# Optimization experiments

Hardware: AMD Instinct MI355X
Metric: run time of the kernel (lower is better)

Reference implementation:

```python
import jax, jax.numpy as jnp
import numpy as np

N_NODES = 100000
N_EDGES = 1600000
D_FEAT = 128
D_OUT = 128


def gcn_conv(x, W, b, src, dst, w, n):
    # symmetric normalization (PyG GCNConv with self-loops already appended)
    deg = jax.ops.segment_sum(w, dst, num_segments=n)
    dinv = jnp.where(deg > 0, jax.lax.rsqrt(deg), 0.0)
    norm = dinv[src] * w * dinv[dst]                       # [E]
    h = x @ W                                              # [N, Dout]
    out = jax.ops.segment_sum(h[src] * norm[:, None], dst, num_segments=n)
    return out + b


def setup_inputs() -> dict:
    key = jax.random.key(0)
    ks = jax.random.split(key, 20)
    feat = jax.random.normal(ks[0], (N_NODES, D_FEAT), dtype=jnp.float32)
    gdv = jax.random.uniform(ks[1], (N_NODES, 73), dtype=jnp.float32)
    pr = jax.random.uniform(ks[2], (N_NODES, 1), dtype=jnp.float32)
    edge_index = jax.random.randint(ks[3], (2, N_EDGES), 0, N_NODES, dtype=jnp.int32)
    edge_weight = jax.random.uniform(ks[4], (N_EDGES,), dtype=jnp.float32)

    def lin(k, fi, fo):
        bound = 1.0 / np.sqrt(fi)
        k1, k2 = jax.random.split(k)
        W = jax.random.uniform(k1, (fi, fo), minval=-bound, maxval=bound, dtype=jnp.float32)
        b = jax.random.uniform(k2, (fo,), minval=-bound, maxval=bound, dtype=jnp.float32)
        return W, b

    W1, b1 = lin(ks[5], D_FEAT, D_OUT)          # gcn_layer1
    W2, b2 = lin(ks[6], D_OUT, D_OUT // 2)      # gcn_layer2
    gdv_W, gdv_b = lin(ks[7], 73, D_OUT // 4)
    pr_W, pr_b = lin(ks[8], 1, D_OUT // 4)
    enc_W1, enc_b1 = lin(ks[9], D_OUT, D_OUT)
    enc_W2, enc_b2 = lin(ks[10], D_OUT, D_OUT)
    return dict(feat=feat, gdv=gdv, pr=pr, edge_index=edge_index, edge_weight=edge_weight,
                W1=W1, b1=b1, W2=W2, b2=b2, gdv_W=gdv_W, gdv_b=gdv_b, pr_W=pr_W, pr_b=pr_b,
                enc_W1=enc_W1, enc_b1=enc_b1, enc_W2=enc_W2, enc_b2=enc_b2)


def reference(feat, gdv, pr, edge_index, edge_weight,
              W1, b1, W2, b2, gdv_W, gdv_b, pr_W, pr_b,
              enc_W1, enc_b1, enc_W2, enc_b2):
    n = feat.shape[0]
    loop = jnp.arange(n, dtype=edge_index.dtype)
    src = jnp.concatenate([edge_index[0], loop])
    dst = jnp.concatenate([edge_index[1], loop])
    w = jnp.concatenate([edge_weight, jnp.ones((n,), dtype=edge_weight.dtype)])

    h = jnp.tanh(gcn_conv(feat, W1, b1, src, dst, w, n))
    adj = jax.nn.sigmoid(gcn_conv(h, W2, b2, src, dst, w, n))   # [N, D/2]

    g = jax.nn.sigmoid(gdv @ gdv_W + gdv_b)                      # [N, D/4]
    p = jax.nn.sigmoid(pr @ pr_W + pr_b)                         # [N, D/4]

    enc = jnp.concatenate([adj, g, p], axis=1)                   # [N, D]
    enc = jnp.tanh(enc @ enc_W1 + enc_b1) @ enc_W2 + enc_b2
    return enc
```

## Files before the change

kernel.cpp:

```cpp
#include <hip/hip_runtime.h>
#include <hip/hip_bf16.h>
#include <cstdint>
#include <cstddef>

#define TPB 256
#define SCAN_CHUNK 1024

typedef short bf16x8 __attribute__((ext_vector_type(8)));
typedef float f32x4 __attribute__((ext_vector_type(4)));

__device__ __forceinline__ float sigmoidf_(float x) {
    return 1.0f / (1.0f + __expf(-x));
}
__device__ __forceinline__ unsigned short f2bf(float x) {
    unsigned u = __float_as_uint(x);
    u += 0x7FFF + ((u >> 16) & 1);
    return (unsigned short)(u >> 16);
}
__device__ __forceinline__ float bf2f(unsigned short b) {
    return __uint_as_float(((unsigned)b) << 16);
}

__device__ __forceinline__ void gld_lds16(const void* gsrc, void* ldst) {
    __builtin_amdgcn_global_load_lds(
        (const __attribute__((address_space(1))) unsigned*)gsrc,
        (__attribute__((address_space(3))) unsigned*)ldst, 16, 0, 0);
}


__global__ __launch_bounds__(TPB) void k_zero(unsigned* counts, int n) {
    int i = blockIdx.x * TPB + threadIdx.x;
    if (i < n) counts[i] = 0u;
}

__global__ __launch_bounds__(TPB) void k_pass1(const int* __restrict__ dst,
                                               unsigned* __restrict__ counts,
                                               unsigned* __restrict__ epos, int E) {
    int e = blockIdx.x * TPB + threadIdx.x;
    if (e < E) epos[e] = atomicAdd(&counts[dst[e]], 1u);
}

__global__ __launch_bounds__(TPB) void k_scan_a(const unsigned* __restrict__ counts,
                                                int* __restrict__ rowptr,
                                                int* __restrict__ bsums, int n) {
    __shared__ int s[SCAN_CHUNK];
    int base = blockIdx.x * SCAN_CHUNK;
    int orig[4];
    #pragma unroll
    for (int j0 = 0; j0 < 4; ++j0) {
        int j = threadIdx.x + j0 * TPB;
        int v = (base + j < n) ? (int)counts[base + j] : 0;
        orig[j0] = v;
        s[j] = v;
    }
    __syncthreads();
    for (int off = 1; off < SCAN_CHUNK; off <<= 1) {
        int t[4];
        #pragma unroll
        for (int j0 = 0; j0 < 4; ++j0) {
            int j = threadIdx.x + j0 * TPB;
            t[j0] = (j >= off) ? s[j - off] : 0;
        }
        __syncthreads();
        #pragma unroll
        for (int j0 = 0; j0 < 4; ++j0) {
            int j = threadIdx.x + j0 * TPB;
            s[j] += t[j0];
        }
        __syncthreads();
    }
    #pragma unroll
    for (int j0 = 0; j0 < 4; ++j0) {
        int j = threadIdx.x + j0 * TPB;
        if (base + j < n) rowptr[base + j] = s[j] - orig[j0];
    }
    if (threadIdx.x == 0) bsums[blockIdx.x] = s[SCAN_CHUNK - 1];
}

__global__ void k_scan_b(int* bsums, int nb) {
    __shared__ int s[128];
    int t = threadIdx.x;
    int v = (t < nb) ? bsums[t] : 0;
    s[t] = v;
    __syncthreads();
    for (int off = 1; off < 128; off <<= 1) {
        int x = (t >= off) ? s[t - off] : 0;
        __syncthreads();
        s[t] += x;
        __syncthreads();
    }
    if (t < nb) bsums[t] = s[t] - v;
}

__global__ __launch_bounds__(TPB) void k_scan_c(int* __restrict__ rowptr,
                                                const int* __restrict__ bsums,
                                                int n, int E) {
    int i = blockIdx.x * TPB + threadIdx.x;
    if (i < n) rowptr[i] += bsums[i / SCAN_CHUNK];
    if (i == 0) rowptr[n] = E;
}

__global__ __launch_bounds__(TPB) void k_fill(const int* __restrict__ src,
                                              const int* __restrict__ dst,
                                              const float* __restrict__ ew,
                                              const int* __restrict__ rowptr,
                                              const unsigned* __restrict__ epos,
                                              int* __restrict__ colIdx,
                                              float* __restrict__ valNorm, int E) {
    int e = blockIdx.x * TPB + threadIdx.x;
    if (e < E) {
        unsigned slot = (unsigned)rowptr[dst[e]] + epos[e];
        colIdx[slot] = src[e];
        valNorm[slot] = ew[e];
    }
}

__global__ __launch_bounds__(TPB) void k_deg(const int* __restrict__ rowptr,
                                             const float* __restrict__ valRaw,
                                             float* __restrict__ dinv, int n) {
    int i = blockIdx.x * TPB + threadIdx.x;
    if (i >= n) return;
    int beg = rowptr[i], end = rowptr[i + 1];
    float s = 1.0f;
    for (int e = beg; e < end; ++e) s += valRaw[e];
    dinv[i] = rsqrtf(s);
}

__global__ __launch_bounds__(TPB) void k_scale(const int* __restrict__ colIdx,
                                               const float* __restrict__ dinv,
                                               float* __restrict__ valNorm, int E) {
    int e = blockIdx.x * TPB + threadIdx.x;
    if (e < E) valNorm[e] *= dinv[colIdx[e]];
}

template<int D, int ACT>
__global__ __launch_bounds__(TPB) void k_agg(const unsigned short* __restrict__ h,
                                             const int* __restrict__ rowptr,
                                             const int* __restrict__ colIdx,
                                             const float* __restrict__ valNorm,
                                             const float* __restrict__ dinv,
                                             const float* __restrict__ bias,
                                             unsigned short* __restrict__ out,
                                             int ldo, int n) {
    const int lane = threadIdx.x & 63;
    const int node = blockIdx.x * 4 + (threadIdx.x >> 6);
    if (node >= n) return;
    constexpr int PER = D / 64;
    float acc[PER];
    const float di = dinv[node];
    if constexpr (PER == 2) {
        unsigned hv = *(const unsigned*)&h[(size_t)node * D + lane * 2];
        acc[0] = bf2f((unsigned short)hv) * di;
        acc[1] = bf2f((unsigned short)(hv >> 16)) * di;
    } else {
        acc[0] = bf2f(h[(size_t)node * D + lane]) * di;
    }
    const int beg = rowptr[node];
    const int end = rowptr[node + 1];
    for (int e = beg; e < end; e += 8) {
        int ss[8]; float nn[8];
        #pragma unroll
        for (int u = 0; u < 8; ++u) {
            int idx = e + u;
            int cl = idx < end ? idx : (end - 1);
            ss[u] = colIdx[cl];
            nn[u] = idx < end ? valNorm[cl] : 0.0f;
        }
        if constexpr (PER == 2) {
            unsigned hv[8];
            #pragma unroll
            for (int u = 0; u < 8; ++u)
                hv[u] = *(const unsigned*)&h[(size_t)ss[u] * D + lane * 2];
            #pragma unroll
            for (int u = 0; u < 8; ++u) {
                acc[0] += bf2f((unsigned short)hv[u]) * nn[u];
                acc[1] += bf2f((unsigned short)(hv[u] >> 16)) * nn[u];
            }
        } else {
            unsigned short hv[8];
            #pragma unroll
            for (int u = 0; u < 8; ++u) hv[u] = h[(size_t)ss[u] * D + lane];
            #pragma unroll
            for (int u = 0; u < 8; ++u) acc[0] += bf2f(hv[u]) * nn[u];
        }
    }
    if constexpr (PER == 2) {
        float v0 = acc[0] * di + bias[lane * 2];
        float v1 = acc[1] * di + bias[lane * 2 + 1];
        if constexpr (ACT == 1) { v0 = tanhf(v0); v1 = tanhf(v1); }
        else                    { v0 = sigmoidf_(v0); v1 = sigmoidf_(v1); }
        unsigned pk = (unsigned)f2bf(v0) | ((unsigned)f2bf(v1) << 16);
        *(unsigned*)&out[(size_t)node * ldo + lane * 2] = pk;
    } else {
        float v = acc[0] * di + bias[lane];
        v = (ACT == 1) ? tanhf(v) : sigmoidf_(v);
        out[(size_t)node * ldo + lane] = f2bf(v);
    }
}

template<int M>
__global__ __launch_bounds__(TPB) void k_prep_w(const float* __restrict__ W,
                                                unsigned short* __restrict__ Wt) {
    int c = blockIdx.x * TPB + threadIdx.x;
    if (c >= M * 16) return;
    int m = c >> 4, k0 = (c & 15) << 3;
    unsigned o[4];
    #pragma unroll
    for (int j = 0; j < 4; ++j) {
        unsigned lo = f2bf(W[(size_t)(k0 + 2 * j) * M + m]);
        unsigned hi = f2bf(W[(size_t)(k0 + 2 * j + 1) * M + m]);
        o[j] = lo | (hi << 16);
    }
    unsigned byte = ((unsigned)c * 16) ^ (unsigned)((m & 7) << 4);
    *(uint4*)((char*)Wt + byte) = *(uint4*)o;
}

template<int M, int ACT, bool A_BF16, bool OUT_F32>
__global__ __launch_bounds__(TPB) void k_mgemm(const void* __restrict__ Ap,
                                               const unsigned short* __restrict__ Wtg,
                                               const float* __restrict__ bias,
                                               void* __restrict__ Cp, int ldc,
                                               int coff, int n) {
    constexpr int K = 128;
    __shared__ __align__(16) unsigned short Al[128 * K];
    __shared__ __align__(16) unsigned short Wt[M * K];

    const int tid = threadIdx.x;
    const int wv = tid >> 6;
    const int ln = tid & 63;
    const int rbase = blockIdx.x * 128;

    constexpr int WCH = (M * K * 2) / 1024;
    #pragma unroll
    for (int c = 0; c < WCH / 4; ++c) {
        int cc = wv * (WCH / 4) + c;
        gld_lds16((const char*)Wtg + cc * 1024 + ln * 16, (char*)Wt + cc * 1024);
    }

    if (A_BF16 && rbase + 128 <= n) {
        #pragma unroll
        for (int it = 0; it < 8; ++it) {
            unsigned dbase = (unsigned)(wv * 8 + it) * 1024;
            unsigned d = dbase + (unsigned)ln * 16;
            unsigned row = d >> 8;
            unsigned s = d ^ ((row & 7) << 4);
            gld_lds16((const char*)Ap + (size_t)rbase * 256 + s, (char*)Al + dbase);
        }
    } else {
        for (int ch = tid; ch < 128 * 16; ch += TPB) {
            int row = ch >> 4;
            int col8 = (ch & 15) * 8;
            int r = rbase + row;
            unsigned o4[4] = {0u, 0u, 0u, 0u};
            if (r < n) {
                if constexpr (A_BF16) {
                    uint4 v = *(const uint4*)((const unsigned short*)Ap + (size_t)r * 128 + col8);
                    o4[0] = v.x; o4[1] = v.y; o4[2] = v.z; o4[3] = v.w;
                } else {
                    float4 a = *(const float4*)((const float*)Ap + (size_t)r * 128 + col8);
                    float4 b = *(const float4*)((const float*)Ap + (size_t)r * 128 + col8 + 4);
                    o4[0] = (unsigned)f2bf(a.x) | ((unsigned)f2bf(a.y) << 16);
                    o4[1] = (unsigned)f2bf(a.z) | ((unsigned)f2bf(a.w) << 16);
                    o4[2] = (unsigned)f2bf(b.x) | ((unsigned)f2bf(b.y) << 16);
                    o4[3] = (unsigned)f2bf(b.z) | ((unsigned)f2bf(b.w) << 16);
                }
            }
            unsigned byte = ((unsigned)ch * 16) ^ (unsigned)((row & 7) << 4);
            *(uint4*)((char*)Al + byte) = *(uint4*)o4;
        }
    }
    __syncthreads();

    const int lr = ln & 15;
    const int lg = ln >> 4;

    constexpr int MF = M / 16;
    f32x4 acc[2][MF];
    #pragma unroll
    for (int i = 0; i < 2; ++i)
        #pragma unroll
        for (int j = 0; j < MF; ++j) acc[i][j] = (f32x4){0.f, 0.f, 0.f, 0.f};

    #pragma unroll
    for (int kk = 0; kk < 4; ++kk) {
        const int kb = kk * 64 + lg * 16;
        bf16x8 af[2];
        #pragma unroll
        for (int rf = 0; rf < 2; ++rf) {
            int row = wv * 32 + rf * 16 + lr;
            unsigned byte = (unsigned)(row * 256 + kb) ^ (unsigned)((row & 7) << 4);
            af[rf] = *(bf16x8*)((char*)Al + byte);
        }
        #pragma unroll
        for (int mf = 0; mf < MF; ++mf) {
            int col = mf * 16 + lr;
            unsigned byte = (unsigned)(col * 256 + kb) ^ (unsigned)((col & 7) << 4);
            bf16x8 bfg = *(bf16x8*)((char*)Wt + byte);
            acc[0][mf] = __builtin_amdgcn_mfma_f32_16x16x32_bf16(af[0], bfg, acc[0][mf], 0, 0, 0);
            acc[1][mf] = __builtin_amdgcn_mfma_f32_16x16x32_bf16(af[1], bfg, acc[1][mf], 0, 0, 0);
        }
    }

    #pragma unroll
    for (int rf = 0; rf < 2; ++rf) {
        #pragma unroll
        for (int j = 0; j < 4; ++j) {
            int row = rbase + wv * 32 + rf * 16 + lg * 4 + j;
            if (row < n) {
                #pragma unroll
                for (int mf = 0; mf < MF; ++mf) {
                    int col = mf * 16 + lr;
                    float v = acc[rf][mf][j] + (bias ? bias[col] : 0.0f);
                    if constexpr (ACT == 1) v = tanhf(v);
                    else if constexpr (ACT == 2) v = sigmoidf_(v);
                    if constexpr (OUT_F32)
                        ((float*)Cp)[(size_t)row * ldc + coff + col] = v;
                    else
                        ((unsigned short*)Cp)[(size_t)row * ldc + coff + col] = f2bf(v);
                }
            }
        }
    }
}

template<int K, int M, int RI>
__global__ __launch_bounds__(TPB) void k_gemm_s(const float* __restrict__ A, int lda,
                                                const float* __restrict__ W,
                                                const float* __restrict__ bias,
                                                unsigned short* __restrict__ C, int ldc,
                                                int coff, int n) {
    constexpr int TPR = M;
    constexpr int G = TPB / TPR;
    constexpr int RT = G * RI;
    __shared__ float Alds[RT * K];
    __shared__ float Wlds[K * M];
    for (int i = threadIdx.x; i < K * M; i += TPB) Wlds[i] = W[i];

    const int c0 = threadIdx.x % TPR;
    const int rg = threadIdx.x / TPR;
    const int rbase = blockIdx.x * RT;

    for (int i = threadIdx.x; i < RT * K; i += TPB) {
        int rr = i / K;
        int r = rbase + rr;
        Alds[i] = (r < n) ? A[(size_t)r * lda + (i - rr * K)] : 0.0f;
    }
    __syncthreads();

    float acc[RI];
    #pragma unroll
    for (int j = 0; j < RI; ++j) acc[j] = 0.0f;
    const float* Ab = &Alds[rg * RI * K];
    #pragma unroll 4
    for (int k = 0; k < K; ++k) {
        float wv = Wlds[k * M + c0];
        #pragma unroll
        for (int j = 0; j < RI; ++j) acc[j] += Ab[j * K + k] * wv;
    }
    #pragma unroll
    for (int j = 0; j < RI; ++j) {
        int r = rbase + rg * RI + j;
        if (r < n) C[(size_t)r * ldc + coff + c0] = f2bf(sigmoidf_(acc[j] + bias[c0]));
    }
}

__global__ __launch_bounds__(TPB) void k_pr(const float* __restrict__ pr,
                                            const float* __restrict__ prW,
                                            const float* __restrict__ prB,
                                            unsigned short* __restrict__ enc, int n) {
    int i = blockIdx.x * TPB + threadIdx.x;
    if (i < n * 32) {
        int node = i >> 5;
        int c = i & 31;
        float v = pr[node] * prW[c] + prB[c];
        enc[(size_t)node * 128 + 96 + c] = f2bf(sigmoidf_(v));
    }
}


extern "C" void kernel_launch(void* const* d_in, const int* in_sizes, int n_in,
                              void* d_out, int out_size, void* d_ws, size_t ws_size,
                              hipStream_t stream) {
    const float* feat = (const float*)d_in[0];
    const float* gdv  = (const float*)d_in[1];
    const float* pr   = (const float*)d_in[2];
    const int*   eidx = (const int*)d_in[3];
    const float* ew   = (const float*)d_in[4];
    const float* W1   = (const float*)d_in[5];
    const float* b1   = (const float*)d_in[6];
    const float* W2   = (const float*)d_in[7];
    const float* b2   = (const float*)d_in[8];
    const float* gdvW = (const float*)d_in[9];
    const float* gdvB = (const float*)d_in[10];
    const float* prW  = (const float*)d_in[11];
    const float* prB  = (const float*)d_in[12];
    const float* eW1  = (const float*)d_in[13];
    const float* eB1  = (const float*)d_in[14];
    const float* eW2  = (const float*)d_in[15];
    const float* eB2  = (const float*)d_in[16];
    float* out = (float*)d_out;

    const int N = in_sizes[0] / 128;
    const int E = in_sizes[4];
    const int* srcA = eidx;
    const int* dstA = eidx + E;

    char* p = (char*)d_ws;
    auto alloc = [&](size_t bytes) {
        char* r = p;
        p += (bytes + 255) & ~(size_t)255;
        return r;
    };
    unsigned* counts  = (unsigned*)alloc((size_t)N * 4);
    unsigned* epos    = (unsigned*)alloc((size_t)E * 4);
    float*    dinv    = (float*)   alloc((size_t)N * 4);
    int*      rowptr  = (int*)     alloc((size_t)(N + 1) * 4);
    int*      bsums   = (int*)     alloc(256 * 4);
    int*      colIdx  = (int*)     alloc((size_t)E * 4);
    float*    valNorm = (float*)   alloc((size_t)E * 4);
    unsigned short* wt1  = (unsigned short*)alloc(128 * 128 * 2);
    unsigned short* wt2  = (unsigned short*)alloc(128 * 64 * 2);
    unsigned short* wtE1 = (unsigned short*)alloc(128 * 128 * 2);
    unsigned short* wtE2 = (unsigned short*)alloc(128 * 128 * 2);
    unsigned short* bufA = (unsigned short*)alloc((size_t)N * 128 * 2);
    unsigned short* bufB = (unsigned short*)alloc((size_t)N * 128 * 2);

    const int nbN = (N + TPB - 1) / TPB;
    const int nbE = (E + TPB - 1) / TPB;
    const int nscan = (N + SCAN_CHUNK - 1) / SCAN_CHUNK;
    const int nbM = (N + 127) / 128;

    k_prep_w<128><<<8, TPB, 0, stream>>>(W1, wt1);
    k_prep_w<64><<<4, TPB, 0, stream>>>(W2, wt2);
    k_prep_w<128><<<8, TPB, 0, stream>>>(eW1, wtE1);
    k_prep_w<128><<<8, TPB, 0, stream>>>(eW2, wtE2);

    k_zero<<<nbN, TPB, 0, stream>>>(counts, N);
    k_pass1<<<nbE, TPB, 0, stream>>>(dstA, counts, epos, E);
    k_scan_a<<<nscan, TPB, 0, stream>>>(counts, rowptr, bsums, N);
    k_scan_b<<<1, 128, 0, stream>>>(bsums, nscan);
    k_scan_c<<<nbN, TPB, 0, stream>>>(rowptr, bsums, N, E);
    k_fill<<<nbE, TPB, 0, stream>>>(srcA, dstA, ew, rowptr, epos, colIdx, valNorm, E);
    k_deg<<<nbN, TPB, 0, stream>>>(rowptr, valNorm, dinv, N);
    k_scale<<<nbE, TPB, 0, stream>>>(colIdx, dinv, valNorm, E);

    k_mgemm<128, 0, false, false><<<nbM, TPB, 0, stream>>>(
        feat, wt1, nullptr, bufA, 128, 0, N);
    k_agg<128, 1><<<(N + 3) / 4, TPB, 0, stream>>>(
        bufA, rowptr, colIdx, valNorm, dinv, b1, bufB, 128, N);
    k_mgemm<64, 0, true, false><<<nbM, TPB, 0, stream>>>(
        bufB, wt2, nullptr, bufA, 64, 0, N);
    k_agg<64, 2><<<(N + 3) / 4, TPB, 0, stream>>>(
        bufA, rowptr, colIdx, valNorm, dinv, b2, bufB, 128, N);
    k_gemm_s<73, 32, 4><<<(N + 31) / 32, TPB, 0, stream>>>(
        gdv, 73, gdvW, gdvB, bufB, 128, 64, N);
    k_pr<<<((size_t)N * 32 + TPB - 1) / TPB, TPB, 0, stream>>>(pr, prW, prB, bufB, N);
    k_mgemm<128, 1, true, false><<<nbM, TPB, 0, stream>>>(
        bufB, wtE1, eB1, bufA, 128, 0, N);
    k_mgemm<128, 0, true, true><<<nbM, TPB, 0, stream>>>(
        bufA, wtE2, eB2, out, 128, 0, N);
}
```

Baseline: 599.7 us.

## Fuse GCN pipeline kernels and pack CSR edges into interleaved index/weight pairs

Merges the weight-prep and counter-zeroing kernels into one launch, runs the first GEMM alongside the edge-counting atomics in a single grid, packs column index and weight into uint2 edge records, and drops the separate edge-scaling pass. It also runs the second aggregation, the gdv linear layer and the pr projection as one heterogeneous grid, and fuses the two encoder GEMMs so the intermediate tile stays in LDS. The aim is fewer launches, less global traffic for the intermediate encoder activations, and gathering each edge's index and weight with one load. The risks are more heterogeneous blocks and higher LDS use in the merged kernels, which may lower occupancy, and the normalization now has to be applied inside aggregation, which is not fully visible here.

Result: faster. 539.6 us (-10.0%).

```diff
diff --git a/kernel.cpp b/kernel.cpp
--- a/kernel.cpp
+++ b/kernel.cpp
@@ -27,181 +27,9 @@
         (__attribute__((address_space(3))) unsigned*)ldst, 16, 0, 0);
 }
 
-
-__global__ __launch_bounds__(TPB) void k_zero(unsigned* counts, int n) {
-    int i = blockIdx.x * TPB + threadIdx.x;
-    if (i < n) counts[i] = 0u;
-}
-
-__global__ __launch_bounds__(TPB) void k_pass1(const int* __restrict__ dst,
-                                               unsigned* __restrict__ counts,
-                                               unsigned* __restrict__ epos, int E) {
-    int e = blockIdx.x * TPB + threadIdx.x;
-    if (e < E) epos[e] = atomicAdd(&counts[dst[e]], 1u);
-}
-
-__global__ __launch_bounds__(TPB) void k_scan_a(const unsigned* __restrict__ counts,
-                                                int* __restrict__ rowptr,
-                                                int* __restrict__ bsums, int n) {
-    __shared__ int s[SCAN_CHUNK];
-    int base = blockIdx.x * SCAN_CHUNK;
-    int orig[4];
-    #pragma unroll
-    for (int j0 = 0; j0 < 4; ++j0) {
-        int j = threadIdx.x + j0 * TPB;
-        int v = (base + j < n) ? (int)counts[base + j] : 0;
-        orig[j0] = v;
-        s[j] = v;
-    }
-    __syncthreads();
-    for (int off = 1; off < SCAN_CHUNK; off <<= 1) {
-        int t[4];
-        #pragma unroll
-        for (int j0 = 0; j0 < 4; ++j0) {
-            int j = threadIdx.x + j0 * TPB;
-            t[j0] = (j >= off) ? s[j - off] : 0;
-        }
-        __syncthreads();
-        #pragma unroll
-        for (int j0 = 0; j0 < 4; ++j0) {
-            int j = threadIdx.x + j0 * TPB;
-            s[j] += t[j0];
-        }
-        __syncthreads();
-    }
-    #pragma unroll
-    for (int j0 = 0; j0 < 4; ++j0) {
-        int j = threadIdx.x + j0 * TPB;
-        if (base + j < n) rowptr[base + j] = s[j] - orig[j0];
-    }
-    if (threadIdx.x == 0) bsums[blockIdx.x] = s[SCAN_CHUNK - 1];
-}
-
-__global__ void k_scan_b(int* bsums, int nb) {
-    __shared__ int s[128];
-    int t = threadIdx.x;
-    int v = (t < nb) ? bsums[t] : 0;
-    s[t] = v;
-    __syncthreads();
-    for (int off = 1; off < 128; off <<= 1) {
-        int x = (t >= off) ? s[t - off] : 0;
-        __syncthreads();
-        s[t] += x;
-        __syncthreads();
-    }
-    if (t < nb) bsums[t] = s[t] - v;
-}
-
-__global__ __launch_bounds__(TPB) void k_scan_c(int* __restrict__ rowptr,
-                                                const int* __restrict__ bsums,
-                                                int n, int E) {
-    int i = blockIdx.x * TPB + threadIdx.x;
-    if (i < n) rowptr[i] += bsums[i / SCAN_CHUNK];
-    if (i == 0) rowptr[n] = E;
-}
-
-__global__ __launch_bounds__(TPB) void k_fill(const int* __restrict__ src,
-                                              const int* __restrict__ dst,
-                                              const float* __restrict__ ew,
-                                              const int* __restrict__ rowptr,
-                                              const unsigned* __restrict__ epos,
-                                              int* __restrict__ colIdx,
-                                              float* __restrict__ valNorm, int E) {
-    int e = blockIdx.x * TPB + threadIdx.x;
-    if (e < E) {
-        unsigned slot = (unsigned)rowptr[dst[e]] + epos[e];
-        colIdx[slot] = src[e];
-        valNorm[slot] = ew[e];
-    }
-}
-
-__global__ __launch_bounds__(TPB) void k_deg(const int* __restrict__ rowptr,
-                                             const float* __restrict__ valRaw,
-                                             float* __restrict__ dinv, int n) {
-    int i = blockIdx.x * TPB + threadIdx.x;
-    if (i >= n) return;
-    int beg = rowptr[i], end = rowptr[i + 1];
-    float s = 1.0f;
-    for (int e = beg; e < end; ++e) s += valRaw[e];
-    dinv[i] = rsqrtf(s);
-}
-
-__global__ __launch_bounds__(TPB) void k_scale(const int* __restrict__ colIdx,
-                                               const float* __restrict__ dinv,
-                                               float* __restrict__ valNorm, int E) {
-    int e = blockIdx.x * TPB + threadIdx.x;
-    if (e < E) valNorm[e] *= dinv[colIdx[e]];
-}
-
-template<int D, int ACT>
-__global__ __launch_bounds__(TPB) void k_agg(const unsigned short* __restrict__ h,
-                                             const int* __restrict__ rowptr,
-                                             const int* __restrict__ colIdx,
-                                             const float* __restrict__ valNorm,
-                                             const float* __restrict__ dinv,
-                                             const float* __restrict__ bias,
-                                             unsigned short* __restrict__ out,
-                                             int ldo, int n) {
-    const int lane = threadIdx.x & 63;
-    const int node = blockIdx.x * 4 + (threadIdx.x >> 6);
-    if (node >= n) return;
-    constexpr int PER = D / 64;
-    float acc[PER];
-    const float di = dinv[node];
-    if constexpr (PER == 2) {
-        unsigned hv = *(const unsigned*)&h[(size_t)node * D + lane * 2];
-        acc[0] = bf2f((unsigned short)hv) * di;
-        acc[1] = bf2f((unsigned short)(hv >> 16)) * di;
-    } else {
-        acc[0] = bf2f(h[(size_t)node * D + lane]) * di;
-    }
-    const int beg = rowptr[node];
-    const int end = rowptr[node + 1];
-    for (int e = beg; e < end; e += 8) {
-        int ss[8]; float nn[8];
-        #pragma unroll
-        for (int u = 0; u < 8; ++u) {
-            int idx = e + u;
-            int cl = idx < end ? idx : (end - 1);
-            ss[u] = colIdx[cl];
-            nn[u] = idx < end ? valNorm[cl] : 0.0f;
-        }
-        if constexpr (PER == 2) {
-            unsigned hv[8];
-            #pragma unroll
-            for (int u = 0; u < 8; ++u)
-                hv[u] = *(const unsigned*)&h[(size_t)ss[u] * D + lane * 2];
-            #pragma unroll
-            for (int u = 0; u < 8; ++u) {
-                acc[0] += bf2f((unsigned short)hv[u]) * nn[u];
-                acc[1] += bf2f((unsigned short)(hv[u] >> 16)) * nn[u];
-            }
-        } else {
-            unsigned short hv[8];
-            #pragma unroll
-            for (int u = 0; u < 8; ++u) hv[u] = h[(size_t)ss[u] * D + lane];
-            #pragma unroll
-            for (int u = 0; u < 8; ++u) acc[0] += bf2f(hv[u]) * nn[u];
-        }
-    }
-    if constexpr (PER == 2) {
-        float v0 = acc[0] * di + bias[lane * 2];
-        float v1 = acc[1] * di + bias[lane * 2 + 1];
-        if constexpr (ACT == 1) { v0 = tanhf(v0); v1 = tanhf(v1); }
-        else                    { v0 = sigmoidf_(v0); v1 = sigmoidf_(v1); }
-        unsigned pk = (unsigned)f2bf(v0) | ((unsigned)f2bf(v1) << 16);
-        *(unsigned*)&out[(size_t)node * ldo + lane * 2] = pk;
-    } else {
-        float v = acc[0] * di + bias[lane];
-        v = (ACT == 1) ? tanhf(v) : sigmoidf_(v);
-        out[(size_t)node * ldo + lane] = f2bf(v);
-    }
-}
-
 template<int M>
-__global__ __launch_bounds__(TPB) void k_prep_w(const float* __restrict__ W,
-                                                unsigned short* __restrict__ Wt) {
-    int c = blockIdx.x * TPB + threadIdx.x;
+__device__ __forceinline__ void prep_w_body(const float* __restrict__ W,
+                                            unsigned short* __restrict__ Wt, int c) {
     if (c >= M * 16) return;
     int m = c >> 4, k0 = (c & 15) << 3;
     unsigned o[4];
@@ -215,22 +43,37 @@
     *(uint4*)((char*)Wt + byte) = *(uint4*)o;
 }
 
+__global__ __launch_bounds__(TPB) void k_prep(const float* W1, unsigned short* wt1,
+                                              const float* W2, unsigned short* wt2,
+                                              const float* E1, unsigned short* wtE1,
+                                              const float* E2, unsigned short* wtE2,
+                                              unsigned* counts, int n, int nbZ) {
+    int bid = blockIdx.x;
+    if (bid < nbZ) {
+        int i = bid * TPB + threadIdx.x;
+        if (i < n) counts[i] = 0u;
+    } else {
+        int t = bid - nbZ;
+        if (t < 8)       prep_w_body<128>(W1, wt1, t * TPB + threadIdx.x);
+        else if (t < 12) prep_w_body<64>(W2, wt2, (t - 8) * TPB + threadIdx.x);
+        else if (t < 20) prep_w_body<128>(E1, wtE1, (t - 12) * TPB + threadIdx.x);
+        else             prep_w_body<128>(E2, wtE2, (t - 20) * TPB + threadIdx.x);
+    }
+}
+
 template<int M, int ACT, bool A_BF16, bool OUT_F32>
-__global__ __launch_bounds__(TPB) void k_mgemm(const void* __restrict__ Ap,
-                                               const unsigned short* __restrict__ Wtg,
-                                               const float* __restrict__ bias,
-                                               void* __restrict__ Cp, int ldc,
-                                               int coff, int n) {
-    constexpr int K = 128;
-    __shared__ __align__(16) unsigned short Al[128 * K];
-    __shared__ __align__(16) unsigned short Wt[M * K];
-
+__device__ __forceinline__ void mgemm_body(const void* __restrict__ Ap,
+                                           const unsigned short* __restrict__ Wtg,
+                                           const float* __restrict__ bias,
+                                           void* __restrict__ Cp, int ldc, int coff,
+                                           int n, int tile,
+                                           unsigned short* Al, unsigned short* Wt) {
     const int tid = threadIdx.x;
     const int wv = tid >> 6;
     const int ln = tid & 63;
-    const int rbase = blockIdx.x * 128;
-
-    constexpr int WCH = (M * K * 2) / 1024;
+    const int rbase = tile * 128;
+
+    constexpr int WCH = (M * 128 * 2) / 1024;
     #pragma unroll
     for (int c = 0; c < WCH / 4; ++c) {
         int cc = wv * (WCH / 4) + c;
@@ -323,57 +166,390 @@
     }
 }
 
-template<int K, int M, int RI>
-__global__ __launch_bounds__(TPB) void k_gemm_s(const float* __restrict__ A, int lda,
-                                                const float* __restrict__ W,
+__global__ __launch_bounds__(TPB) void k_g1p1(const float* __restrict__ feat,
+                                              const unsigned short* __restrict__ wt1,
+                                              unsigned short* __restrict__ bufA,
+                                              int n, int nbM,
+                                              const int* __restrict__ dst,
+                                              unsigned* __restrict__ counts,
+                                              unsigned* __restrict__ epos, int E) {
+    __shared__ __align__(16) unsigned short Al[128 * 128];
+    __shared__ __align__(16) unsigned short Wt[128 * 128];
+    if (blockIdx.x < nbM) {
+        mgemm_body<128, 0, false, false>(feat, wt1, nullptr, bufA, 128, 0, n,
+                                         blockIdx.x, Al, Wt);
+    } else {
+        int e = (blockIdx.x - nbM) * TPB + threadIdx.x;
+        if (e < E) epos[e] = atomicAdd(&counts[dst[e]], 1u);
+    }
+}
+
+__global__ __launch_bounds__(TPB) void k_mgemm64(const unsigned short* __restrict__ Ap,
+                                                 const unsigned short* __restrict__ Wtg,
+                                                 unsigned short* __restrict__ Cp, int n) {
+    __shared__ __align__(16) unsigned short Al[128 * 128];
+    __shared__ __align__(16) unsigned short Wt[64 * 128];
+    mgemm_body<64, 0, true, false>(Ap, Wtg, nullptr, Cp, 64, 0, n, blockIdx.x, Al, Wt);
+}
+
+__global__ __launch_bounds__(TPB) void k_enc2(const unsigned short* __restrict__ enc,
+                                              const unsigned short* __restrict__ w1g,
+                                              const float* __restrict__ b1,
+                                              const unsigned short* __restrict__ w2g,
+                                              const float* __restrict__ b2,
+                                              float* __restrict__ out, int n) {
+    __shared__ __align__(16) unsigned short Al[128 * 128];
+    __shared__ __align__(16) unsigned short Wt[128 * 128];
+    const int tid = threadIdx.x;
+    const int wv = tid >> 6;
+    const int ln = tid & 63;
+    const int rbase = blockIdx.x * 128;
+    const int lr = ln & 15;
+    const int lg = ln >> 4;
+
+    #pragma unroll
+    for (int c = 0; c < 8; ++c) {
+        int cc = wv * 8 + c;
+        gld_lds16((const char*)w1g + cc * 1024 + ln * 16, (char*)Wt + cc * 1024);
+    }
+    if (rbase + 128 <= n) {
+        #pragma unroll
+        for (int it = 0; it < 8; ++it) {
+            unsigned dbase = (unsigned)(wv * 8 + it) * 1024;
+            unsigned d = dbase + (unsigned)ln * 16;
+            unsigned row = d >> 8;
+            unsigned s = d ^ ((row & 7) << 4);
+            gld_lds16((const char*)enc + (size_t)rbase * 256 + s, (char*)Al + dbase);
+        }
+    } else {
+        for (int ch = tid; ch < 128 * 16; ch += TPB) {
+            int row = ch >> 4;
+            int col8 = (ch & 15) * 8;
+            int r = rbase + row;
+            unsigned o4[4] = {0u, 0u, 0u, 0u};
+            if (r < n) {
+                uint4 v = *(const uint4*)(enc + (size_t)r * 128 + col8);
+                o4[0] = v.x; o4[1] = v.y; o4[2] = v.z; o4[3] = v.w;
+            }
+            unsigned byte = ((unsigned)ch * 16) ^ (unsigned)((row & 7) << 4);
+            *(uint4*)((char*)Al + byte) = *(uint4*)o4;
+        }
+    }
+    __syncthreads();
+
+    f32x4 acc[2][8];
+    #pragma unroll
+    for (int i = 0; i < 2; ++i)
+        #pragma unroll
+        for (int j = 0; j < 8; ++j) acc[i][j] = (f32x4){0.f, 0.f, 0.f, 0.f};
+
+    #pragma unroll
+    for (int kk = 0; kk < 4; ++kk) {
+        const int kb = kk * 64 + lg * 16;
+        bf16x8 af[2];
+        #pragma unroll
+        for (int rf = 0; rf < 2; ++rf) {
+            int row = wv * 32 + rf * 16 + lr;
+            unsigned byte = (unsigned)(row * 256 + kb) ^ (unsigned)((row & 7) << 4);
+            af[rf] = *(bf16x8*)((char*)Al + byte);
+        }
+        #pragma unroll
+        for (int mf = 0; mf < 8; ++mf) {
+            int col = mf * 16 + lr;
+            unsigned byte = (unsigned)(col * 256 + kb) ^ (unsigned)((col & 7) << 4);
+            bf16x8 bfg = *(bf16x8*)((char*)Wt + byte);
+            acc[0][mf] = __builtin_amdgcn_mfma_f32_16x16x32_bf16(af[0], bfg, acc[0][mf], 0, 0, 0);
+            acc[1][mf] = __builtin_amdgcn_mfma_f32_16x16x32_bf16(af[1], bfg, acc[1][mf], 0, 0, 0);
+        }
+    }
+    __syncthreads();
+
+    #pragma unroll
+    for (int c = 0; c < 8; ++c) {
+        int cc = wv * 8 + c;
+        gld_lds16((const char*)w2g + cc * 1024 + ln * 16, (char*)Wt + cc * 1024);
+    }
+    #pragma unroll
+    for (int rf = 0; rf < 2; ++rf) {
+        #pragma unroll
+        for (int j = 0; j < 4; ++j) {
+            int rl = wv * 32 + rf * 16 + lg * 4 + j;
+            #pragma unroll
+            for (int mf = 0; mf < 8; ++mf) {
+                int col = mf * 16 + lr;
+                float v = tanhf(acc[rf][mf][j] + b1[col]);
+                unsigned byte = (unsigned)(rl * 256 + col * 2) ^ (unsigned)((rl & 7) << 4);
+                *(unsigned short*)((char*)Al + byte) = f2bf(v);
+            }
+        }
+    }
+    __syncthreads();
+
+    #pragma unroll
+    for (int i = 0; i < 2; ++i)
+        #pragma unroll
+        for (int j = 0; j < 8; ++j) acc[i][j] = (f32x4){0.f, 0.f, 0.f, 0.f};
+
+    #pragma unroll
+    for (int kk = 0; kk < 4; ++kk) {
+        const int kb = kk * 64 + lg * 16;
+        bf16x8 af[2];
+        #pragma unroll
+        for (int rf = 0; rf < 2; ++rf) {
+            int row = wv * 32 + rf * 16 + lr;
+            unsigned byte = (unsigned)(row * 256 + kb) ^ (unsigned)((row & 7) << 4);
+            af[rf] = *(bf16x8*)((char*)Al + byte);
+        }
+        #pragma unroll
+        for (int mf = 0; mf < 8; ++mf) {
+            int col = mf * 16 + lr;
+            unsigned byte = (unsigned)(col * 256 + kb) ^ (unsigned)((col & 7) << 4);
+            bf16x8 bfg = *(bf16x8*)((char*)Wt + byte);
+            acc[0][mf] = __builtin_amdgcn_mfma_f32_16x16x32_bf16(af[0], bfg, acc[0][mf], 0, 0, 0);
+            acc[1][mf] = __builtin_amdgcn_mfma_f32_16x16x32_bf16(af[1], bfg, acc[1][mf], 0, 0, 0);
+        }
+    }
+
+    #pragma unroll
+    for (int rf = 0; rf < 2; ++rf) {
+        #pragma unroll
+        for (int j = 0; j < 4; ++j) {
+            int row = rbase + wv * 32 + rf * 16 + lg * 4 + j;
+            if (row < n) {
+                #pragma unroll
+                for (int mf = 0; mf < 8; ++mf) {
+                    int col = mf * 16 + lr;
+                    out[(size_t)row * 128 + col] = acc[rf][mf][j] + b2[col];
+                }
+            }
+        }
+    }
+}
+
+
+__global__ __launch_bounds__(TPB) void k_scan_a(const unsigned* __restrict__ counts,
+                                                int* __restrict__ rowptr,
+                                                int* __restrict__ bsums, int n) {
+    __shared__ int s[SCAN_CHUNK];
+    int base = blockIdx.x * SCAN_CHUNK;
+    int orig[4];
+    #pragma unroll
+    for (int j0 = 0; j0 < 4; ++j0) {
+        int j = threadIdx.x + j0 * TPB;
+        int v = (base + j < n) ? (int)counts[base + j] : 0;
+        orig[j0] = v;
+        s[j] = v;
+    }
+    __syncthreads();
+    for (int off = 1; off < SCAN_CHUNK; off <<= 1) {
+        int t[4];
+        #pragma unroll
+        for (int j0 = 0; j0 < 4; ++j0) {
+            int j = threadIdx.x + j0 * TPB;
+            t[j0] = (j >= off) ? s[j - off] : 0;
+        }
+        __syncthreads();
+        #pragma unroll
+        for (int j0 = 0; j0 < 4; ++j0) {
+            int j = threadIdx.x + j0 * TPB;
+            s[j] += t[j0];
+        }
+        __syncthreads();
+    }
+    #pragma unroll
+    for (int j0 = 0; j0 < 4; ++j0) {
+        int j = threadIdx.x + j0 * TPB;
+        if (base + j < n) rowptr[base + j] = s[j] - orig[j0];
+    }
+    if (threadIdx.x == 0) bsums[blockIdx.x] = s[SCAN_CHUNK - 1];
+}
+
+__global__ void k_scan_b(int* bsums, int nb) {
+    __shared__ int s[128];
+    int t = threadIdx.x;
+    int v = (t < nb) ? bsums[t] : 0;
+    s[t] = v;
+    __syncthreads();
+    for (int off = 1; off < 128; off <<= 1) {
+        int x = (t >= off) ? s[t - off] : 0;
+        __syncthreads();
+        s[t] += x;
+        __syncthreads();
+    }
+    if (t < nb) bsums[t] = s[t] - v;
+}
+
+__global__ __launch_bounds__(TPB) void k_scan_c(int* __restrict__ rowptr,
+                                                const int* __restrict__ bsums,
+                                                int n, int E) {
+    int i = blockIdx.x * TPB + threadIdx.x;
+    if (i < n) rowptr[i] += bsums[i / SCAN_CHUNK];
+    if (i == 0) rowptr[n] = E;
+}
+
+__global__ __launch_bounds__(TPB) void k_fill(const int* __restrict__ src,
+                                              const int* __restrict__ dst,
+                                              const float* __restrict__ ew,
+                                              const int* __restrict__ rowptr,
+                                              const unsigned* __restrict__ epos,
+                                              uint2* __restrict__ edges, int E) {
+    int e = blockIdx.x * TPB + threadIdx.x;
+    if (e < E) {
+        unsigned slot = (unsigned)rowptr[dst[e]] + epos[e];
+        uint2 pk;
+        pk.x = (unsigned)src[e];
+        pk.y = __float_as_uint(ew[e]);
+        edges[slot] = pk;
+    }
+}
+
+__global__ __launch_bounds__(TPB) void k_deg(const int* __restrict__ rowptr,
+                                             const uint2* __restrict__ edges,
+                                             float* __restrict__ dinv, int n) {
+    int i = blockIdx.x * TPB + threadIdx.x;
+    if (i >= n) return;
+    int beg = rowptr[i], end = rowptr[i + 1];
+    float s = 1.0f;
+    for (int e = beg; e < end; ++e) s += __uint_as_float(edges[e].y);
+    dinv[i] = rsqrtf(s);
+}
+
+template<int D, int ACT>
+__device__ __forceinline__ void agg_body(const unsigned short* __restrict__ h,
+                                         const int* __restrict__ rowptr,
+                                         const uint2* __restrict__ edges,
+                                         const float* __restrict__ dinv,
+                                         const float* __restrict__ bias,
+                                         unsigned short* __restrict__ out,
+                                         int ldo, int n, int node) {
+    const int lane = threadIdx.x & 63;
+    constexpr int PER = D / 64;
+    float acc[PER];
+    const float di = dinv[node];
+    if constexpr (PER == 2) {
+        unsigned hv = *(const unsigned*)&h[(size_t)node * D + lane * 2];
+        acc[0] = bf2f((unsigned short)hv) * di;
+        acc[1] = bf2f((unsigned short)(hv >> 16)) * di;
+    } else {
+        acc[0] = bf2f(h[(size_t)node * D + lane]) * di;
+    }
+    const int beg = rowptr[node];
+    const int end = rowptr[node + 1];
+    for (int e = beg; e < end; e += 8) {
+        int ss[8]; float ww[8];
+        #pragma unroll
+        for (int u = 0; u < 8; ++u) {
+            int idx = e + u;
+            int cl = idx < end ? idx : (end - 1);
+            uint2 ed = edges[cl];
+            ss[u] = (int)ed.x;
+            ww[u] = idx < end ? __uint_as_float(ed.y) : 0.0f;
+        }
+        float nn[8];
+        #pragma unroll
+        for (int u = 0; u < 8; ++u) nn[u] = ww[u] * dinv[ss[u]];
+        if constexpr (PER == 2) {
+            unsigned hv[8];
+            #pragma unroll
+            for (int u = 0; u < 8; ++u)
+                hv[u] = *(const unsigned*)&h[(size_t)ss[u] * D + lane * 2];
+            #pragma unroll
+            for (int u = 0; u < 8; ++u) {
+                acc[0] += bf2f((unsigned short)hv[u]) * nn[u];
+                acc[1] += bf2f((unsigned short)(hv[u] >> 16)) * nn[u];
+            }
+        } else {
+            unsigned short hv[8];
+            #pragma unroll
+            for (int u = 0; u < 8; ++u) hv[u] = h[(size_t)ss[u] * D + lane];
+            #pragma unroll
+            for (int u = 0; u < 8; ++u) acc[0] += bf2f(hv[u]) * nn[u];
+        }
+    }
+    if constexpr (PER == 2) {
+        float v0 = acc[0] * di + bias[lane * 2];
+        float v1 = acc[1] * di + bias[lane * 2 + 1];
+        if constexpr (ACT == 1) { v0 = tanhf(v0); v1 = tanhf(v1); }
+        else                    { v0 = sigmoidf_(v0); v1 = sigmoidf_(v1); }
+        unsigned pk = (unsigned)f2bf(v0) | ((unsigned)f2bf(v1) << 16);
+        *(unsigned*)&out[(size_t)node * ldo + lane * 2] = pk;
+    } else {
+        float v = acc[0] * di + bias[lane];
+        v = (ACT == 1) ? tanhf(v) : sigmoidf_(v);
+        out[(size_t)node * ldo + lane] = f2bf(v);
+    }
+}
+
+__global__ __launch_bounds__(TPB) void k_agg128(const unsigned short* __restrict__ h,
+                                                const int* __restrict__ rowptr,
+                                                const uint2* __restrict__ edges,
+                                                const float* __restrict__ dinv,
                                                 const float* __restrict__ bias,
-                                                unsigned short* __restrict__ C, int ldc,
-                                                int coff, int n) {
-    constexpr int TPR = M;
-    constexpr int G = TPB / TPR;
-    constexpr int RT = G * RI;
-    __shared__ float Alds[RT * K];
-    __shared__ float Wlds[K * M];
-    for (int i = threadIdx.x; i < K * M; i += TPB) Wlds[i] = W[i];
-
-    const int c0 = threadIdx.x % TPR;
-    const int rg = threadIdx.x / TPR;
-    const int rbase = blockIdx.x * RT;
-
-    for (int i = threadIdx.x; i < RT * K; i += TPB) {
-        int rr = i / K;
+                                                unsigned short* __restrict__ out, int n) {
+    int node = blockIdx.x * 4 + (threadIdx.x >> 6);
+    if (node < n) agg_body<128, 1>(h, rowptr, edges, dinv, bias, out, 128, n, node);
+}
+
+__device__ __forceinline__ void gemm_s_body(const float* __restrict__ A,
+                                            const float* __restrict__ W,
+                                            const float* __restrict__ bias,
+                                            unsigned short* __restrict__ C,
+                                            int n, int tile,
+                                            float* Alds, float* Wlds) {
+    for (int i = threadIdx.x; i < 73 * 32; i += TPB) Wlds[i] = W[i];
+    const int c0 = threadIdx.x & 31;
+    const int rg = threadIdx.x >> 5;
+    const int rbase = tile * 32;
+    for (int i = threadIdx.x; i < 32 * 73; i += TPB) {
+        int rr = i / 73;
         int r = rbase + rr;
-        Alds[i] = (r < n) ? A[(size_t)r * lda + (i - rr * K)] : 0.0f;
+        Alds[i] = (r < n) ? A[(size_t)r * 73 + (i - rr * 73)] : 0.0f;
     }
     __syncthreads();
-
-    float acc[RI];
-    #pragma unroll
-    for (int j = 0; j < RI; ++j) acc[j] = 0.0f;
-    const float* Ab = &Alds[rg * RI * K];
+    float acc[4] = {0.f, 0.f, 0.f, 0.f};
+    const float* Ab = &Alds[rg * 4 * 73];
     #pragma unroll 4
-    for (int k = 0; k < K; ++k) {
-        float wv = Wlds[k * M + c0];
-        #pragma unroll
-        for (int j = 0; j < RI; ++j) acc[j] += Ab[j * K + k] * wv;
-    }
-    #pragma unroll
-    for (int j = 0; j < RI; ++j) {
-        int r = rbase + rg * RI + j;
-        if (r < n) C[(size_t)r * ldc + coff + c0] = f2bf(sigmoidf_(acc[j] + bias[c0]));
-    }
-}
-
-__global__ __launch_bounds__(TPB) void k_pr(const float* __restrict__ pr,
-                                            const float* __restrict__ prW,
-                                            const float* __restrict__ prB,
-                                            unsigned short* __restrict__ enc, int n) {
-    int i = blockIdx.x * TPB + threadIdx.x;
-    if (i < n * 32) {
-        int node = i >> 5;
-        int c = i & 31;
-        float v = pr[node] * prW[c] + prB[c];
-        enc[(size_t)node * 128 + 96 + c] = f2bf(sigmoidf_(v));
+    for (int k = 0; k < 73; ++k) {
+        float wv = Wlds[k * 32 + c0];
+        #pragma unroll
+        for (int j = 0; j < 4; ++j) acc[j] += Ab[j * 73 + k] * wv;
+    }
+    #pragma unroll
+    for (int j = 0; j < 4; ++j) {
+        int r = rbase + rg * 4 + j;
+        if (r < n) C[(size_t)r * 128 + 64 + c0] = f2bf(sigmoidf_(acc[j] + bias[c0]));
+    }
+}
+
+__global__ __launch_bounds__(TPB) void k_tail(const unsigned short* __restrict__ h2,
+                                              const int* __restrict__ rowptr,
+                                              const uint2* __restrict__ edges,
+                                              const float* __restrict__ dinv,
+                                              const float* __restrict__ b2,
+                                              unsigned short* __restrict__ enc,
+                                              const float* __restrict__ gdv,
+                                              const float* __restrict__ gdvW,
+                                              const float* __restrict__ gdvB,
+                                              const float* __restrict__ pr,
+                                              const float* __restrict__ prW,
+                                              const float* __restrict__ prB,
+                                              int n, int nA, int nG) {
+    __shared__ float Alds[32 * 73];
+    __shared__ float Wlds[73 * 32];
+    int bid = blockIdx.x;
+    if (bid < nA) {
+        int node = bid * 4 + (threadIdx.x >> 6);
+        if (node < n) agg_body<64, 2>(h2, rowptr, edges, dinv, b2, enc, 128, n, node);
+    } else if (bid < nA + nG) {
+        gemm_s_body(gdv, gdvW, gdvB, enc, n, bid - nA, Alds, Wlds);
+    } else {
+        int i = (bid - nA - nG) * TPB + threadIdx.x;
+        if (i < n * 32) {
+            int node = i >> 5;
+            int c = i & 31;
+            float v = pr[node] * prW[c] + prB[c];
+            enc[(size_t)node * 128 + 96 + c] = f2bf(sigmoidf_(v));
+        }
     }
 }
 
@@ -411,13 +587,12 @@
         p += (bytes + 255) & ~(size_t)255;
         return r;
     };
-    unsigned* counts  = (unsigned*)alloc((size_t)N * 4);
-    unsigned* epos    = (unsigned*)alloc((size_t)E * 4);
-    float*    dinv    = (float*)   alloc((size_t)N * 4);
-    int*      rowptr  = (int*)     alloc((size_t)(N + 1) * 4);
-    int*      bsums   = (int*)     alloc(256 * 4);
-    int*      colIdx  = (int*)     alloc((size_t)E * 4);
-    float*    valNorm = (float*)   alloc((size_t)E * 4);
+    unsigned* counts = (unsigned*)alloc((size_t)N * 4);
+    unsigned* epos   = (unsigned*)alloc((size_t)E * 4);
+    float*    dinv   = (float*)   alloc((size_t)N * 4);
+    int*      rowptr = (int*)     alloc((size_t)(N + 1) * 4);
+    int*      bsums  = (int*)     alloc(256 * 4);
+    uint2*    edges  = (uint2*)   alloc((size_t)E * 8);
     unsigned short* wt1  = (unsigned short*)alloc(128 * 128 * 2);
     unsigned short* wt2  = (unsigned short*)alloc(128 * 64 * 2);
     unsigned short* wtE1 = (unsigned short*)alloc(128 * 128 * 2);
@@ -429,34 +604,22 @@
     const int nbE = (E + TPB - 1) / TPB;
     const int nscan = (N + SCAN_CHUNK - 1) / SCAN_CHUNK;
     const int nbM = (N + 127) / 128;
-
-    k_prep_w<128><<<8, TPB, 0, stream>>>(W1, wt1);
-    k_prep_w<64><<<4, TPB, 0, stream>>>(W2, wt2);
-    k_prep_w<128><<<8, TPB, 0, stream>>>(eW1, wtE1);
-    k_prep_w<128><<<8, TPB, 0, stream>>>(eW2, wtE2);
-
-    k_zero<<<nbN, TPB, 0, stream>>>(counts, N);
-    k_pass1<<<nbE, TPB, 0, stream>>>(dstA, counts, epos, E);
+    const int nA = (N + 3) / 4;
+    const int nG = (N + 31) / 32;
+    const int nP = (N * 32 + TPB - 1) / TPB;
+
+    k_prep<<<nbN + 28, TPB, 0, stream>>>(W1, wt1, W2, wt2, eW1, wtE1, eW2, wtE2,
+                                         counts, N, nbN);
+    k_g1p1<<<nbM + nbE, TPB, 0, stream>>>(feat, wt1, bufA, N, nbM,
+                                          dstA, counts, epos, E);
     k_scan_a<<<nscan, TPB, 0, stream>>>(counts, rowptr, bsums, N);
     k_scan_b<<<1, 128, 0, stream>>>(bsums, nscan);
     k_scan_c<<<nbN, TPB, 0, stream>>>(rowptr, bsums, N, E);
-    k_fill<<<nbE, TPB, 0, stream>>>(srcA, dstA, ew, rowptr, epos, colIdx, valNorm, E);
-    k_deg<<<nbN, TPB, 0, stream>>>(rowptr, valNorm, dinv, N);
-    k_scale<<<nbE, TPB, 0, stream>>>(colIdx, dinv, valNorm, E);
-
-    k_mgemm<128, 0, false, false><<<nbM, TPB, 0, stream>>>(
-        feat, wt1, nullptr, bufA, 128, 0, N);
-    k_agg<128, 1><<<(N + 3) / 4, TPB, 0, stream>>>(
-        bufA, rowptr, colIdx, valNorm, dinv, b1, bufB, 128, N);
-    k_mgemm<64, 0, true, false><<<nbM, TPB, 0, stream>>>(
-        bufB, wt2, nullptr, bufA, 64, 0, N);
-    k_agg<64, 2><<<(N + 3) / 4, TPB, 0, stream>>>(
-        bufA, rowptr, colIdx, valNorm, dinv, b2, bufB, 128, N);
-    k_gemm_s<73, 32, 4><<<(N + 31) / 32, TPB, 0, stream>>>(
-        gdv, 73, gdvW, gdvB, bufB, 128, 64, N);
-    k_pr<<<((size_t)N * 32 + TPB - 1) / TPB, TPB, 0, stream>>>(pr, prW, prB, bufB, N);
-    k_mgemm<128, 1, true, false><<<nbM, TPB, 0, stream>>>(
-        bufB, wtE1, eB1, bufA, 128, 0, N);
-    k_mgemm<128, 0, true, true><<<nbM, TPB, 0, stream>>>(
-        bufA, wtE2, eB2, out, 128, 0, N);
-}
+    k_fill<<<nbE, TPB, 0, stream>>>(srcA, dstA, ew, rowptr, epos, edges, E);
+    k_deg<<<nbN, TPB, 0, stream>>>(rowptr, edges, dinv, N);
+    k_agg128<<<nA, TPB, 0, stream>>>(bufA, rowptr, edges, dinv, b1, bufB, N);
+    k_mgemm64<<<nbM, TPB, 0, stream>>>(bufB, wt2, bufA, N);
+    k_tail<<<nA + nG + nP, TPB, 0, stream>>>(bufA, rowptr, edges, dinv, b2, bufB,
+                                             gdv, gdvW, gdvB, pr, prW, prB, N, nA, nG);
+    k_enc2<<<nbM, TPB, 0, stream>>>(bufB, wtE1, eB1, wtE2, eB2, out, N);
+}
```
